# Optimization experiments

Hardware: AMD Instinct MI355X
Metric: run time of the kernel (lower is better)

Reference implementation:

```python
import jax, jax.numpy as jnp
import numpy as np

N_BLOCKS = 16
N_FEATS = 64
SCALE = 2
RGB_RANGE = 255.0
RGB_MEAN = np.array([0.4488, 0.4371, 0.4040], dtype=np.float32)  # DIV2K mean used by EDSR MeanShift


def conv2d(x, w, b=None):
    # x: [N,C,H,W], w: [O,I,kh,kw], SAME padding, stride 1
    y = jax.lax.conv_general_dilated(x, w, (1, 1), 'SAME',
                                     dimension_numbers=('NCHW', 'OIHW', 'NCHW'))
    if b is not None:
        y = y + b[None, :, None, None]
    return y


def ste_sign(x):
    # sign with straight-through estimator (identity gradient)
    return x + jax.lax.stop_gradient(jnp.sign(x) - x)


def bin_conv(x, w):
    # XNOR-style 1-bit conv: binarize activations to {-1,+1} (sign, STE),
    # binarize weights to sign(w) * alpha where alpha = per-output-channel mean(|w|).
    xb = ste_sign(x)
    alpha = jnp.mean(jnp.abs(w), axis=(1, 2, 3), keepdims=True)  # [O,1,1,1]
    wb = ste_sign(w) * alpha
    return conv2d(xb, wb)


def pixel_shuffle(x, r):
    # torch nn.PixelShuffle semantics
    n, c, h, w = x.shape
    x = x.reshape(n, c // (r * r), r, r, h, w)
    x = x.transpose(0, 1, 4, 2, 5, 3)  # [n, c', h, r, w, r]
    return x.reshape(n, c // (r * r), h * r, w * r)


def setup_inputs() -> dict:
    key = jax.random.key(0)
    ks = jax.random.split(key, 8)
    fan = 1.0 / np.sqrt(N_FEATS * 9)
    x = jax.random.uniform(ks[0], (16, 3, 128, 128), jnp.float32) * RGB_RANGE
    w_head = jax.random.normal(ks[1], (N_FEATS, 3, 3, 3), jnp.float32) * (1.0 / np.sqrt(3 * 9))
    w_body = jax.random.normal(ks[2], (N_BLOCKS, 2, N_FEATS, N_FEATS, 3, 3), jnp.float32) * fan
    w_body_last = jax.random.normal(ks[3], (N_FEATS, N_FEATS, 3, 3), jnp.float32) * fan
    w_up = jax.random.normal(ks[4], (N_FEATS * SCALE * SCALE, N_FEATS, 3, 3), jnp.float32) * fan
    w_tail = jax.random.normal(ks[5], (3, N_FEATS, 3, 3), jnp.float32) * fan
    b_tail = jnp.zeros((3,), jnp.float32)
    return {'x': x, 'w_head': w_head, 'w_body': w_body, 'w_body_last': w_body_last,
            'w_up': w_up, 'w_tail': w_tail, 'b_tail': b_tail}


def reference(x, w_head, w_body, w_body_last, w_up, w_tail, b_tail):
    shift = jnp.asarray(RGB_RANGE * RGB_MEAN).reshape(1, 3, 1, 1)
    x = x - shift                      # sub_mean
    h = conv2d(x, w_head)              # full-precision head, [N,64,H,W]
    r = h
    for i in range(N_BLOCKS):          # fixed layer count
        t = bin_conv(r, w_body[i, 0])
        t = jnp.tanh(t)
        t = bin_conv(t, w_body[i, 1])
        r = r + t                      # res_scale = 1
    r = bin_conv(r, w_body_last)
    res = r + h                        # global skip; this is `out`
    t = conv2d(res, w_up)              # 64 -> 64*r^2
    t = pixel_shuffle(t, SCALE)        # [N,64,H*r,W*r]
    t = conv2d(t, w_tail, b_tail)      # 64 -> 3
    out_img = t + shift                # add_mean
    return (out_img, res)
```

## Files before the change

kernel.cpp:

```cpp
#include <hip/hip_runtime.h>
#include <stdint.h>

typedef unsigned long long u64;
typedef unsigned int u32;
typedef _Float16 f16;
using i32x4  = __attribute__((ext_vector_type(4))) int;
using i32x16 = __attribute__((ext_vector_type(16))) int;
using f32x2  = __attribute__((ext_vector_type(2))) float;
using f32x4  = __attribute__((ext_vector_type(4))) float;
using f16x4  = __attribute__((ext_vector_type(4))) _Float16;

#define HW 16384

#define OFF_R      0ull
#define OFF_WEFF2  35651584ull
#define OFF_SG0    67108864ull
#define OFF_SG1    69206016ull
#define OFF_NZT    71303168ull
#define OFF_WBSG   73400320ull
#define OFF_ALPHA  74616832ull
#define OFF_WEFF   74625280ull

__global__ __launch_bounds__(256) void k_prep_wbsg(const float* __restrict__ wbody, const float* __restrict__ wlast,
                                                   signed char* __restrict__ wB, float* __restrict__ alpha){
  int t = blockIdx.x*256 + threadIdx.x;
  if (t >= 33*9*64) return;
  int o = t & 63, tap = (t>>6)%9, cid = t/(64*9);
  const float* src = (cid < 32) ? (wbody + (size_t)cid*36864) : wlast;
  u32 d[16];
  #pragma unroll
  for (int c4=0;c4<16;c4++){
    u32 v=0;
    #pragma unroll
    for (int j=0;j<4;j++){
      float w = src[(o*64 + c4*4+j)*9 + tap];
      v |= ((w < 0.f) ? 0xFFu : 0x01u) << (8*j);
    }
    d[c4]=v;
  }
  i32x4* dst = (i32x4*)(wB + ((size_t)(cid*9+tap)*64 + o)*64);
  #pragma unroll
  for (int k=0;k<4;k++){ i32x4 v; v[0]=(int)d[4*k]; v[1]=(int)d[4*k+1]; v[2]=(int)d[4*k+2]; v[3]=(int)d[4*k+3]; dst[k]=v; }
  if (tap==0){
    float s=0.f;
    for (int ci=0;ci<64;ci++)
      #pragma unroll
      for (int tp=0;tp<9;tp++) s += fabsf(src[(o*64+ci)*9+tp]);
    alpha[cid*64+o] = s * (1.0f/576.0f);
  }
}

__global__ __launch_bounds__(256) void k_prep_weff(const float* __restrict__ wup, const float* __restrict__ wtail,
                                                   float* __restrict__ weff){
  int idx = blockIdx.x*256 + threadIdx.x;
  int rx = idx & 3;
  int px = (idx >> 2) & 1;
  int base = idx >> 3;
  int o  = base % 3;
  int t2 = base / 3;
  int ci = t2 & 63;
  int ry = (t2 >> 6) & 3;
  int py = (t2 >> 8) & 1;
  int e  = t2 >> 9;
  int ex = e % 3, ey = e / 3;
  int ry_off = (py - 2) + ry;
  int rx_off = (px - 2) + rx;
  float acc = 0.f;
  for (int dy=0; dy<3; dy++){
    if (ey==1 && dy==0) continue;
    if (ey==2 && dy==2) continue;
    int pydy = py + dy - 1;
    int sy = ((pydy + 4) >> 1) - 2;
    int vy = (pydy + 4) & 1;
    int a = ry_off + 1 - sy;
    if (a < 0 || a > 2) continue;
    for (int dx=0; dx<3; dx++){
      if (ex==0 && dx==0) continue;
      if (ex==2 && dx==2) continue;
      int pxdx = px + dx - 1;
      int sx = ((pxdx + 4) >> 1) - 2;
      int vx = (pxdx + 4) & 1;
      int b = rx_off + 1 - sx;
      if (b < 0 || b > 2) continue;
      for (int c=0; c<64; c++){
        int u = c*4 + vy*2 + vx;
        acc += wtail[((o*64+c)*3+dy)*3+dx] * wup[((u*64+ci)*3+a)*3+b];
      }
    }
  }
  weff[idx] = acc;
}

__global__ __launch_bounds__(256) void k_prep_repack(const float* __restrict__ weff, float* __restrict__ w2){
  int t = blockIdx.x*256 + threadIdx.x;
  int px = t & 1;
  int q  = t >> 1;
  int rx = q & 3;  q >>= 2;
  int o  = q % 3;  q /= 3;
  int ry = q & 3;  q >>= 2;
  int ci = q & 63;
  int py = q >> 6;
  w2[t] = weff[(size_t)(2+py)*6144 + ry*1536 + ci*24 + (o*2+px)*4 + rx];
}

__global__ __launch_bounds__(256) void k_head(const float* __restrict__ x, const float* __restrict__ wh,
                                              f16* __restrict__ r, float* __restrict__ h, u64* __restrict__ sgR){
  __shared__ float wl[64*27];
  for (int j=threadIdx.x; j<64*27; j+=256) wl[j] = wh[j];
  __syncthreads();
  const int id = blockIdx.x*256 + threadIdx.x;
  const int n = id >> 14, p = id & 16383;
  const int yy = p >> 7, xx = p & 127;
  float xv[27];
  const float sh[3] = {114.444f, 111.4605f, 103.02f};
  #pragma unroll
  for (int tap=0; tap<9; tap++){
    int Yq = yy + tap/3 - 1, Xq = xx + tap%3 - 1;
    bool v = ((unsigned)Yq < 128u) && ((unsigned)Xq < 128u);
    int q = (Yq << 7) + Xq;
    #pragma unroll
    for (int c=0; c<3; c++)
      xv[c*9+tap] = v ? (x[(size_t)(n*3+c)*HW + q] - sh[c]) : 0.f;
  }
  u64 sg = 0;
  for (int o=0; o<64; o++){
    float acc = 0.f;
    #pragma unroll
    for (int j=0; j<27; j++) acc += wl[o*27+j] * xv[j];
    f16 rv = (f16)acc;
    r[(size_t)(n*64+o)*HW + p] = rv;
    h[(size_t)(n*64+o)*HW + p] = acc;
    sg |= (u64)((float)rv < 0.f) << o;
  }
  sgR[id] = sg;
}

template<int MODE>
__global__ __launch_bounds__(256) void k_bconv(const u64* __restrict__ sgIn, const u64* __restrict__ nzIn,
                                               const signed char* __restrict__ wB, const float* __restrict__ alphaC,
                                               f16* __restrict__ rbuf, u64* __restrict__ sgOut,
                                               u64* __restrict__ nzOut, float* __restrict__ resbuf){
  __shared__ signed char Abytes[4*68*80];

  const int bx = blockIdx.x;
  const int n  = bx >> 7;
  const int rem = bx & 127;
  const int y0 = (rem >> 1) << 1;
  const int x0 = (rem & 1) << 6;

  const int lane = threadIdx.x & 63;
  const int wid  = threadIdx.x >> 6;
  const int rrow = wid >> 1;
  const int och  = wid & 1;
  const int nn   = lane & 31;
  const int q    = lane >> 5;

  i32x4 Bf[9][2];
  #pragma unroll
  for (int t=0;t<9;t++)
    #pragma unroll
    for (int h=0;h<2;h++)
      Bf[t][h] = *(const i32x4*)(wB + ((size_t)(t*64 + och*32 + nn))*64 + h*32 + q*16);

  for (int s = threadIdx.x; s < 4*66; s += 256){
    int g = s/66, c = s%66;
    int y = y0 + g - 1, xcol = x0 + c - 1;
    u64 pos=0, neg=0;
    if (((unsigned)y < 128u) && ((unsigned)xcol < 128u)){
      int p = (n<<14) + (y<<7) + xcol;
      u64 sg = sgIn[p];
      if (MODE==1){ u64 nz = nzIn[p]; pos = nz & ~sg; neg = nz & sg; }
      else        { pos = ~sg;        neg = sg; }
    }
    u32 plo=(u32)pos, phi=(u32)(pos>>32), nlo=(u32)neg, nhi=(u32)(neg>>32);
    u32 tmp[16];
    #pragma unroll
    for (int i=0;i<16;i++){
      u32 np = ((i<8) ? (plo >> (4*i)) : (phi >> (4*i-32))) & 0xFu;
      u32 nm = ((i<8) ? (nlo >> (4*i)) : (nhi >> (4*i-32))) & 0xFu;
      u32 bp = (np * 0x00204081u) & 0x01010101u;
      u32 bn = (nm * 0x00204081u) & 0x01010101u;
      tmp[i] = bp | (bn * 0xFFu);
    }
    i32x4* dst = (i32x4*)&Abytes[(g*68 + c)*80];
    #pragma unroll
    for (int k=0;k<4;k++){ i32x4 v; v[0]=(int)tmp[4*k]; v[1]=(int)tmp[4*k+1]; v[2]=(int)tmp[4*k+2]; v[3]=(int)tmp[4*k+3]; dst[k]=v; }
  }
  __syncthreads();

  const float al = (MODE==0) ? 0.f : alphaC[och*32 + nn];

  for (int xh=0; xh<2; xh++){
    i32x16 acc;
    #pragma unroll
    for (int k=0;k<16;k++) acc[k]=0;

    const i32x4* Ap = (const i32x4*)&Abytes[(rrow*68 + xh*32 + nn)*80 + q*16];
    #pragma unroll
    for (int dy=0;dy<3;dy++)
      #pragma unroll
      for (int dx=0;dx<3;dx++){
        const int t = dy*3+dx;
        #pragma unroll
        for (int h=0;h<2;h++){
          i32x4 a = Ap[(dy*68+dx)*5 + h*2];
          acc = __builtin_amdgcn_mfma_i32_32x32x32_i8(a, Bf[t][h], acc, 0, 0, 0);
        }
      }

    const int ybase = y0 + rrow, xbase = x0 + xh*32;

    if (MODE==0){
      u32 sgc=0, nzc=0;
      #pragma unroll
      for (int reg=0; reg<16; reg++){
        u64 bs = __ballot(acc[reg] < 0);
        u64 bn = __ballot(acc[reg] != 0);
        const int px0 = (reg&3) + ((reg>>2)<<3);
        sgc = (lane==px0  ) ? (u32)bs       : sgc;
        sgc = (lane==px0+4) ? (u32)(bs>>32) : sgc;
        nzc = (lane==px0  ) ? (u32)bn       : nzc;
        nzc = (lane==px0+4) ? (u32)(bn>>32) : nzc;
      }
      if (lane < 32){
        int p = (n<<14) + (ybase<<7) + xbase + lane;
        ((u32*)sgOut)[p*2 + och] = sgc;
        ((u32*)nzOut)[p*2 + och] = nzc;
      }
    } else if (MODE==1){
      float newr[16];
      f16* rp = rbuf + ((size_t)((n<<6) + och*32 + nn))*HW + (ybase<<7) + xbase;
      #pragma unroll
      for (int k2=0;k2<4;k2++){
        f16x4 rv4 = *(f16x4*)(rp + 4*q + 8*k2);
        #pragma unroll
        for (int j=0;j<4;j++){
          float rv = (float)rv4[j] + al * (float)acc[4*k2+j];
          rv4[j] = (f16)rv;
          newr[4*k2+j] = (float)rv4[j];
        }
        *(f16x4*)(rp + 4*q + 8*k2) = rv4;
      }
      u32 sgc=0;
      #pragma unroll
      for (int reg=0; reg<16; reg++){
        u64 b = __ballot(newr[reg] < 0.f);
        const int px0 = (reg&3) + ((reg>>2)<<3);
        sgc = (lane==px0  ) ? (u32)b       : sgc;
        sgc = (lane==px0+4) ? (u32)(b>>32) : sgc;
      }
      if (lane < 32){
        int p = (n<<14) + (ybase<<7) + xbase + lane;
        ((u32*)sgOut)[p*2 + och] = sgc;
      }
    } else {
      float* hp = resbuf + ((size_t)((n<<6) + och*32 + nn))*HW + (ybase<<7) + xbase;
      #pragma unroll
      for (int k2=0;k2<4;k2++){
        f32x4 hv = *(f32x4*)(hp + 4*q + 8*k2);
        #pragma unroll
        for (int j=0;j<4;j++) hv[j] += al * (float)acc[4*k2+j];
        *(f32x4*)(hp + 4*q + 8*k2) = hv;
      }
    }
  }
}

__global__ __launch_bounds__(256) void k_tail(const float* __restrict__ res, const float* __restrict__ w2,
                                              const float* __restrict__ btail, float* __restrict__ out){
  __shared__ float wsm[6144];
  __shared__ f32x2 red[128][13];
  const int id  = blockIdx.x;
  const int xcd = id & 7;
  const int t   = id >> 3;
  const int n   = xcd*2 + (t & 1);
  const int py  = (t >> 1) & 1;
  const int yg  = t >> 2;
  const int y0  = yg << 2;
  const int x   = threadIdx.x & 127;
  const int ch  = threadIdx.x >> 7;
  const int rbase = y0 + py - 2;

  {
    const f32x4* src = (const f32x4*)(w2 + (size_t)py*6144);
    f32x4* dst = (f32x4*)wsm;
    #pragma unroll
    for (int j=0;j<6;j++) dst[threadIdx.x + 256*j] = src[threadIdx.x + 256*j];
  }

  int xo[5]; float cm[5];
  #pragma unroll
  for (int j=0;j<5;j++){
    int c = x - 2 + j;
    cm[j] = ((unsigned)c < 128u) ? 1.f : 0.f;
    xo[j] = c < 0 ? 0 : (c > 127 ? 127 : c);
  }

  f32x2 acc[4][3];
  #pragma unroll
  for (int k=0;k<4;k++)
    #pragma unroll
    for (int o=0;o<3;o++) acc[k][o] = (f32x2)(0.f);

  __syncthreads();

  const float* rbn = res + (size_t)n*64*HW;
  const int ci0 = ch*32;
  #pragma unroll 1
  for (int ci=ci0; ci<ci0+32; ci++){
    const float* rp = rbn + (size_t)ci*HW;
    float v[7][5];
    #pragma unroll
    for (int w=0; w<7; w++){
      const int row = rbase + w;
      if ((unsigned)row < 128u){
        const float* q = rp + (row<<7);
        #pragma unroll
        for (int j=0;j<5;j++) v[w][j] = q[xo[j]] * cm[j];
      } else {
        #pragma unroll
        for (int j=0;j<5;j++) v[w][j] = 0.f;
      }
    }
    const float* wp = wsm + ci*96;
    #pragma unroll
    for (int ry=0; ry<4; ry++){
      const float* wr = wp + ry*24;
      f32x4 wq[6];
      #pragma unroll
      for (int j=0;j<6;j++) wq[j] = *(const f32x4*)(wr + 4*j);
      #pragma unroll
      for (int k=0;k<4;k++){
        const float* vv = v[k+ry];
        #pragma unroll
        for (int o=0;o<3;o++){
          #pragma unroll
          for (int rx=0;rx<4;rx++){
            const f32x4 wq4 = wq[o*2 + (rx>>1)];
            f32x2 wv; wv[0]=wq4[(rx&1)*2]; wv[1]=wq4[(rx&1)*2+1];
            f32x2 vp; vp[0]=vv[rx]; vp[1]=vv[rx+1];
            acc[k][o] = __builtin_elementwise_fma(wv, vp, acc[k][o]);
          }
        }
      }
    }
  }

  if (ch==1){
    #pragma unroll
    for (int k=0;k<4;k++)
      #pragma unroll
      for (int o=0;o<3;o++) red[x][k*3+o] = acc[k][o];
  }
  __syncthreads();
  if (ch==0){
    const float sh[3] = {114.444f, 111.4605f, 103.02f};
    #pragma unroll
    for (int k=0;k<4;k++){
      const int Y = ((y0 + k) << 1) + py;
      #pragma unroll
      for (int o=0;o<3;o++){
        f32x2 s2 = acc[k][o] + red[x][k*3+o];
        const float b = btail[o] + sh[o];
        s2[0] += b; s2[1] += b;
        *(f32x2*)(out + (((size_t)((n*3+o)*256 + Y)) << 8) + 2*x) = s2;
      }
    }
  }
}

__global__ __launch_bounds__(256) void k_border(const float* __restrict__ res, const float* __restrict__ weff,
                                                const float* __restrict__ btail, float* __restrict__ out){
  int t = blockIdx.x*256 + threadIdx.x;
  if (t >= 16384) return;
  int n    = t >> 10;
  int rem  = t & 1023;
  int edge = rem >> 8;
  int pos  = rem & 255;
  int X, Y;
  if (edge==0){ Y = 0;   X = pos; if (X==0 || X==255) return; }
  else if (edge==1){ Y = 255; X = pos; if (X==0 || X==255) return; }
  else if (edge==2){ X = 0;   Y = pos; }
  else            { X = 255; Y = pos; }
  int px = X & 1, x = X >> 1;
  int py = Y & 1, y = Y >> 1;
  int ey = (Y==0) ? 1 : ((Y==255) ? 2 : 0);
  int ex = (X==0) ? 0 : ((X==255) ? 2 : 1);
  const float* Ws = weff + (size_t)((ey*3+ex)*2+py) * 6144;
  float acc[3] = {0.f,0.f,0.f};
  for (int ry=0; ry<4; ry++){
    int yy = y + (py-2) + ry;
    bool rowv = ((unsigned)yy < 128u);
    const float* rp = res + (size_t)n*64*HW + yy*128;
    for (int ci=0; ci<64; ci++){
      const float* Wc = Ws + ry*1536 + ci*24 + px*4;
      #pragma unroll
      for (int rx=0; rx<4; rx++){
        int xxc = x + (px-2) + rx;
        float v = (rowv && (unsigned)xxc < 128u) ? rp[(size_t)ci*HW + xxc] : 0.f;
        acc[0] += Wc[0*8+rx] * v;
        acc[1] += Wc[1*8+rx] * v;
        acc[2] += Wc[2*8+rx] * v;
      }
    }
  }
  const float sh[3] = {114.444f, 111.4605f, 103.02f};
  for (int o=0; o<3; o++)
    out[(size_t)((n*3+o)*256+Y)*256 + X] = acc[o] + btail[o] + sh[o];
}

extern "C" void kernel_launch(void* const* d_in, const int* in_sizes, int n_in,
                              void* d_out, int out_size, void* d_ws, size_t ws_size,
                              hipStream_t stream) {
  const float* x      = (const float*)d_in[0];
  const float* w_head = (const float*)d_in[1];
  const float* w_body = (const float*)d_in[2];
  const float* w_last = (const float*)d_in[3];
  const float* w_up   = (const float*)d_in[4];
  const float* w_tail = (const float*)d_in[5];
  const float* b_tail = (const float*)d_in[6];

  char* ws = (char*)d_ws;
  f16*  r      = (f16*) (ws + OFF_R);
  u64*  sg0    = (u64*) (ws + OFF_SG0);
  u64*  sg1    = (u64*) (ws + OFF_SG1);
  u64*  nzT    = (u64*) (ws + OFF_NZT);
  signed char* wBsg = (signed char*)(ws + OFF_WBSG);
  float* alpha = (float*)(ws + OFF_ALPHA);
  float* weff  = (float*)(ws + OFF_WEFF);
  float* weff2 = (float*)(ws + OFF_WEFF2);

  float* out = (float*)d_out;
  float* res = out + 3145728;

  k_prep_wbsg<<<75, 256, 0, stream>>>(w_body, w_last, wBsg, alpha);
  k_prep_weff<<<432, 256, 0, stream>>>(w_up, w_tail, weff);
  k_prep_repack<<<48, 256, 0, stream>>>(weff, weff2);
  k_head<<<1024, 256, 0, stream>>>(x, w_head, r, res, sg0);
  for (int i=0; i<16; i++){
    k_bconv<0><<<2048, 256, 0, stream>>>(sg0, nullptr, wBsg + (size_t)(2*i)*36864,
                                         nullptr, nullptr, sg1, nzT, nullptr);
    k_bconv<1><<<2048, 256, 0, stream>>>(sg1, nzT, wBsg + (size_t)(2*i+1)*36864,
                                         alpha + (2*i+1)*64, r, sg0, nullptr, nullptr);
  }
  k_bconv<2><<<2048, 256, 0, stream>>>(sg0, nullptr, wBsg + (size_t)32*36864,
                                       alpha + 32*64, nullptr, nullptr, nullptr, res);
  k_tail<<<1024, 256, 0, stream>>>(res, weff2, b_tail, out);
  k_border<<<64, 256, 0, stream>>>(res, weff, b_tail, out);
}
```

Baseline: 1.291 ms.

## Store residual stream channel-last and stage head outputs through shared memory

The head kernel now buffers its outputs in shared memory, so the fp32 h write is coalesced per channel and the f16 residual r is written in pixel-major, channel-last layout using 8-wide vector stores. The MODE==1 binary-conv epilogue is changed to index r in the new NHWC layout, which turns its residual update into scalar, 64-element-strided loads and stores. The upsample kernel pre-packs its input and weight pairs into f32x2 registers so the packed FMAs need less register shuffling. Any other reader of r (not shown) has to agree with the new layout, and the strided scalar accesses in the epilogue may cost more than the old vector accesses.

Measured after the change: 1.306 ms. About the same (+1.2%).

```diff
diff --git a/kernel.cpp b/kernel.cpp
--- a/kernel.cpp
+++ b/kernel.cpp
@@ -9,6 +9,7 @@
 using f32x2  = __attribute__((ext_vector_type(2))) float;
 using f32x4  = __attribute__((ext_vector_type(4))) float;
 using f16x4  = __attribute__((ext_vector_type(4))) _Float16;
+using f16x8  = __attribute__((ext_vector_type(8))) _Float16;
 
 #define HW 16384
 
@@ -106,10 +107,12 @@
 __global__ __launch_bounds__(256) void k_head(const float* __restrict__ x, const float* __restrict__ wh,
                                               f16* __restrict__ r, float* __restrict__ h, u64* __restrict__ sgR){
   __shared__ float wl[64*27];
+  __shared__ float hs[32][257];
   for (int j=threadIdx.x; j<64*27; j+=256) wl[j] = wh[j];
-  __syncthreads();
-  const int id = blockIdx.x*256 + threadIdx.x;
+  const int tid = threadIdx.x;
+  const int id = blockIdx.x*256 + tid;
   const int n = id >> 14, p = id & 16383;
+  const int pix0 = (blockIdx.x*256) & 16383;
   const int yy = p >> 7, xx = p & 127;
   float xv[27];
   const float sh[3] = {114.444f, 111.4605f, 103.02f};
@@ -122,15 +125,37 @@
     for (int c=0; c<3; c++)
       xv[c*9+tap] = v ? (x[(size_t)(n*3+c)*HW + q] - sh[c]) : 0.f;
   }
+  __syncthreads();
   u64 sg = 0;
-  for (int o=0; o<64; o++){
-    float acc = 0.f;
-    #pragma unroll
-    for (int j=0; j<27; j++) acc += wl[o*27+j] * xv[j];
-    f16 rv = (f16)acc;
-    r[(size_t)(n*64+o)*HW + p] = rv;
-    h[(size_t)(n*64+o)*HW + p] = acc;
-    sg |= (u64)((float)rv < 0.f) << o;
+  for (int R=0; R<2; R++){
+    for (int o2=0; o2<32; o2++){
+      const int o = R*32 + o2;
+      float acc = 0.f;
+      #pragma unroll
+      for (int j=0; j<27; j++) acc += wl[o*27+j] * xv[j];
+      f16 rv = (f16)acc;
+      sg |= (u64)((float)rv < 0.f) << o;
+      hs[o2][tid] = acc;
+    }
+    __syncthreads();
+    {
+      float* hb = h + (size_t)(n*64 + R*32)*HW + pix0 + tid;
+      #pragma unroll
+      for (int c2=0;c2<32;c2++) hb[(size_t)c2*HW] = hs[c2][tid];
+    }
+    {
+      f16* rb = r + ((size_t)n*HW + pix0)*64 + R*32;
+      #pragma unroll
+      for (int j=0;j<4;j++){
+        int L = j*256 + tid;
+        int pix = L >> 2, c0 = (L & 3)*8;
+        f16x8 t8;
+        #pragma unroll
+        for (int i=0;i<8;i++) t8[i] = (f16)hs[c0+i][pix];
+        *(f16x8*)(rb + (size_t)pix*64 + c0) = t8;
+      }
+    }
+    __syncthreads();
   }
   sgR[id] = sg;
 }
@@ -229,17 +254,18 @@
       }
     } else if (MODE==1){
       float newr[16];
-      f16* rp = rbuf + ((size_t)((n<<6) + och*32 + nn))*HW + (ybase<<7) + xbase;
+      f16* rp = rbuf + ((size_t)n*HW + (ybase<<7) + xbase + 4*q)*64 + och*32 + nn;
       #pragma unroll
       for (int k2=0;k2<4;k2++){
-        f16x4 rv4 = *(f16x4*)(rp + 4*q + 8*k2);
         #pragma unroll
         for (int j=0;j<4;j++){
-          float rv = (float)rv4[j] + al * (float)acc[4*k2+j];
-          rv4[j] = (f16)rv;
-          newr[4*k2+j] = (float)rv4[j];
+          const int po = (8*k2 + j)*64;
+          f16 old = rp[po];
+          float rv = (float)old + al * (float)acc[4*k2+j];
+          f16 nv = (f16)rv;
+          rp[po] = nv;
+          newr[4*k2+j] = (float)nv;
         }
-        *(f16x4*)(rp + 4*q + 8*k2) = rv4;
       }
       u32 sgc=0;
       #pragma unroll
@@ -322,25 +348,29 @@
         for (int j=0;j<5;j++) v[w][j] = 0.f;
       }
     }
+    f32x2 vp[7][4];
+    #pragma unroll
+    for (int w=0; w<7; w++)
+      #pragma unroll
+      for (int rx=0; rx<4; rx++){ vp[w][rx][0] = v[w][rx]; vp[w][rx][1] = v[w][rx+1]; }
     const float* wp = wsm + ci*96;
     #pragma unroll
     for (int ry=0; ry<4; ry++){
       const float* wr = wp + ry*24;
-      f32x4 wq[6];
-      #pragma unroll
-      for (int j=0;j<6;j++) wq[j] = *(const f32x4*)(wr + 4*j);
+      f32x2 wpair[12];
+      #pragma unroll
+      for (int jj=0;jj<6;jj++){
+        f32x4 t4 = *(const f32x4*)(wr + 4*jj);
+        wpair[2*jj][0]   = t4[0]; wpair[2*jj][1]   = t4[1];
+        wpair[2*jj+1][0] = t4[2]; wpair[2*jj+1][1] = t4[3];
+      }
       #pragma unroll
       for (int k=0;k<4;k++){
-        const float* vv = v[k+ry];
         #pragma unroll
         for (int o=0;o<3;o++){
           #pragma unroll
-          for (int rx=0;rx<4;rx++){
-            const f32x4 wq4 = wq[o*2 + (rx>>1)];
-            f32x2 wv; wv[0]=wq4[(rx&1)*2]; wv[1]=wq4[(rx&1)*2+1];
-            f32x2 vp; vp[0]=vv[rx]; vp[1]=vv[rx+1];
-            acc[k][o] = __builtin_elementwise_fma(wv, vp, acc[k][o]);
-          }
+          for (int rx=0;rx<4;rx++)
+            acc[k][o] = __builtin_elementwise_fma(wpair[o*4+rx], vp[k+ry][rx], acc[k][o]);
         }
       }
     }
```
